# Performance work log

Hardware: AMD Instinct MI355X
Metric: run time of the kernel (lower is better)

## Reference

```python
import jax, jax.numpy as jnp
import numpy as np

NUM_GEMMS = 64      # local experts (num_gemms)
IN_SIZE = 2048      # input_size == config.hidden_size (column parallel)
OUT_SIZE = 1408     # per-expert output width
TOTAL_TOKENS = 32768


def setup_inputs() -> dict:
    key = jax.random.key(0)
    kx, kw = jax.random.split(key)
    x = jax.random.normal(kx, (TOTAL_TOKENS, IN_SIZE), dtype=jnp.float32)
    # torch params are [output_size, input_size] per expert -> stack to [E, out, in]
    W = jax.random.normal(kw, (NUM_GEMMS, OUT_SIZE, IN_SIZE), dtype=jnp.float32) * 0.02
    # uneven per-expert row splits, sum == TOTAL_TOKENS (avg 512, alternating 256/768)
    m_splits = jnp.array([256, 768] * (NUM_GEMMS // 2), dtype=jnp.int32)
    return {"x": x, "W": W, "m_splits": m_splits}


def reference(x, W, m_splits):
    # original: original_weight = cat([w.t() for w in weights]) -> [E*in, out]
    # column mode: view(E, hidden, -1) -> [E, in, out]; gmm over row splits.
    w = jnp.transpose(W, (0, 2, 1))  # [E, in, out]
    splits = np.asarray(m_splits)    # row splits are static metadata of the grouped GEMM
    offs = np.concatenate([[0], np.cumsum(splits)])
    # grouped GEMM: out[rows_of_e] = x[rows_of_e] @ w[e]; loop is over the fixed expert set
    outs = [x[offs[e]:offs[e + 1]] @ w[e] for e in range(w.shape[0])]
    return jnp.concatenate(outs, axis=0)  # [total_tokens, out]
```

## Files before the change

kernel.cpp:

```cpp
#include <hip/hip_runtime.h>
#include <hip/hip_bf16.h>

#define E_ 64
#define K_ 2048
#define N_ 1408
#define BM 256
#define BN 128
#define BK 32
#define NK (K_ / BK)
#define NTHREADS 512
#define NTILE (N_ / BN)
#define LDSA (BM * BK * 2)
#define LDSB (BN * BK * 2)
#define LDSBUF (LDSA + LDSB)
#define GRID_ 2112

using f32x4  = __attribute__((ext_vector_type(4))) float;
using bf16x8 = __attribute__((ext_vector_type(8))) short;

#define BAR() asm volatile("s_waitcnt lgkmcnt(0)\n\ts_barrier" ::: "memory")

__device__ __forceinline__ short f2b(float f) {
  __hip_bfloat16 h = __float2bfloat16(f);
  return __builtin_bit_cast(short, h);
}

__global__ void build_meta(const int* __restrict__ m_splits, int* __restrict__ meta) {
  const int e = threadIdx.x;
  const int m = m_splits[e];
  const int mt = (m + BM - 1) / BM;
  int sm = m, smt = mt;
#pragma unroll
  for (int d = 1; d < 64; d <<= 1) {
    const int vm = __shfl_up(sm, d);
    const int vt = __shfl_up(smt, d);
    if (e >= d) { sm += vm; smt += vt; }
  }
  meta[1 + e] = smt - mt;
  meta[66 + e] = sm - m;
  if (e == 63) { meta[1 + 64] = smt; meta[0] = smt * NTILE; }
}

struct Stage { f32x4 a[2][2]; f32x4 b[2]; };

__global__ __launch_bounds__(NTHREADS, 2) void gemm_grouped(
    const float* __restrict__ x, const float* __restrict__ W,
    const int* __restrict__ m_splits, const int* __restrict__ meta,
    float* __restrict__ out) {
  __shared__ char smem[2 * LDSBUF];

  const int J = meta[0];
  const int xcd = blockIdx.x & 7;
  const int pos = blockIdx.x >> 3;
  const int q = J >> 3, r = J & 7;
  if (pos >= q + (xcd < r ? 1 : 0)) return;
  const int jidx = xcd * q + min(xcd, r) + pos;

  int lo = 0, hi = 64;
  while (hi - lo > 1) {
    const int mid = (lo + hi) >> 1;
    if (meta[1 + mid] * NTILE <= jidx) lo = mid; else hi = mid;
  }
  const int e = lo;
  const int mt_e = meta[1 + e + 1] - meta[1 + e];
  const int rem = jidx - meta[1 + e] * NTILE;
  const int nt = rem / mt_e;
  const int t  = rem - nt * mt_e;
  const int m_e = m_splits[e];
  const int row0 = meta[66 + e] + t * BM;
  const int nrows = min(BM, m_e - t * BM);
  const int n0 = nt * BN;

  const int tid  = threadIdx.x;
  const int lane = tid & 63;
  const int w    = tid >> 6;
  const int wm   = w >> 1;
  const int wn   = w & 1;

  const int strow = tid >> 2;
  const int skc8  = (tid & 3) * 8;
  const int kcb   = (tid & 3) * 16;

  const float* xrow = x + (size_t)row0 * K_;
  const float* wrow = W + ((size_t)e * N_ + (size_t)n0) * K_;
  const f32x4 zero4 = {0.f, 0.f, 0.f, 0.f};

  auto load_tiles = [&](int kt, Stage& st) {
    const int kbase = kt * BK + skc8;
#pragma unroll
    for (int c = 0; c < 2; ++c) {
      const int rr = c * 128 + strow;
      if (rr < nrows) {
        const float* pp = xrow + (size_t)rr * K_ + kbase;
        st.a[c][0] = *(const f32x4*)pp;
        st.a[c][1] = *(const f32x4*)(pp + 4);
      } else { st.a[c][0] = zero4; st.a[c][1] = zero4; }
    }
    const float* qq = wrow + (size_t)strow * K_ + kbase;
    st.b[0] = *(const f32x4*)qq;
    st.b[1] = *(const f32x4*)(qq + 4);
  };

  auto write_lds = [&](int buf, const Stage& st) {
    const int base = buf * LDSBUF;
#pragma unroll
    for (int c = 0; c < 2; ++c) {
      const int rr = c * 128 + strow;
      const int off = rr * 64 + (kcb ^ (((rr >> 1) & 3) << 4));
      bf16x8 v;
#pragma unroll
      for (int i = 0; i < 4; ++i) { v[i] = f2b(st.a[c][0][i]); v[i + 4] = f2b(st.a[c][1][i]); }
      *(bf16x8*)(smem + base + off) = v;
    }
    {
      const int rr = strow;
      const int off = rr * 64 + (kcb ^ (((rr >> 1) & 3) << 4));
      bf16x8 v;
#pragma unroll
      for (int i = 0; i < 4; ++i) { v[i] = f2b(st.b[0][i]); v[i + 4] = f2b(st.b[1][i]); }
      *(bf16x8*)(smem + base + LDSA + off) = v;
    }
  };

  f32x4 acc[4][4];
#pragma unroll
  for (int i = 0; i < 4; ++i)
#pragma unroll
    for (int j = 0; j < 4; ++j) acc[i][j] = zero4;

  const int arow0 = wm * 64 + (lane & 15);
  const int brow0 = wn * 64 + (lane & 15);
  const int kslot = (lane >> 4) * 16;

  auto compute = [&](int buf) {
    const int base = buf * LDSBUF;
    bf16x8 af[4], bfr[4];
#pragma unroll
    for (int i = 0; i < 4; ++i) {
      const int rr = arow0 + i * 16;
      af[i] = *(const bf16x8*)(smem + base + rr * 64 + (kslot ^ (((rr >> 1) & 3) << 4)));
    }
#pragma unroll
    for (int j = 0; j < 4; ++j) {
      const int rr = brow0 + j * 16;
      bfr[j] = *(const bf16x8*)(smem + base + LDSA + rr * 64 + (kslot ^ (((rr >> 1) & 3) << 4)));
    }
#pragma unroll
    for (int i = 0; i < 4; ++i)
#pragma unroll
      for (int j = 0; j < 4; ++j)
        acc[i][j] = __builtin_amdgcn_mfma_f32_16x16x32_bf16(af[i], bfr[j], acc[i][j], 0, 0, 0);
  };

  Stage sA;
  load_tiles(0, sA);
  write_lds(0, sA);
  int cur = 0;
  for (int kt = 0; kt < NK; ++kt) {
    if (kt + 1 < NK) load_tiles(kt + 1, sA);
    BAR();
    compute(cur);
    if (kt + 1 < NK) write_lds(cur ^ 1, sA);
    cur ^= 1;
  }

  const int crow = wm * 64 + (lane >> 4) * 4;
  const int ccol = n0 + wn * 64 + (lane & 15);
#pragma unroll
  for (int i = 0; i < 4; ++i) {
#pragma unroll
    for (int rr = 0; rr < 4; ++rr) {
      const int lr = crow + i * 16 + rr;
      if (lr < nrows) {
#pragma unroll
        for (int j = 0; j < 4; ++j)
          out[(size_t)(row0 + lr) * N_ + ccol + j * 16] = acc[i][j][rr];
      }
    }
  }
}

extern "C" void kernel_launch(void* const* d_in, const int* in_sizes, int n_in,
                              void* d_out, int out_size, void* d_ws, size_t ws_size,
                              hipStream_t stream) {
  const float* x        = (const float*)d_in[0];
  const float* W        = (const float*)d_in[1];
  const int*   m_splits = (const int*)d_in[2];
  float*       out      = (float*)d_out;

  int* meta = (int*)d_ws;

  build_meta<<<1, 64, 0, stream>>>(m_splits, meta);
  gemm_grouped<<<GRID_, NTHREADS, 0, stream>>>(x, W, m_splits, meta, out);
}
```

Measured before the change: 385.2 us.

## Shrink M tile to 128 and remap warps to a 2x4 grid

Measured after the change: 449.6 us. 16.7% more time.

```diff
diff --git a/kernel.cpp b/kernel.cpp
--- a/kernel.cpp
+++ b/kernel.cpp
@@ -4,7 +4,7 @@
 #define E_ 64
 #define K_ 2048
 #define N_ 1408
-#define BM 256
+#define BM 128
 #define BN 128
 #define BK 32
 #define NK (K_ / BK)
@@ -13,7 +13,7 @@
 #define LDSA (BM * BK * 2)
 #define LDSB (BN * BK * 2)
 #define LDSBUF (LDSA + LDSB)
-#define GRID_ 2112
+#define GRID_ 3520
 
 using f32x4  = __attribute__((ext_vector_type(4))) float;
 using bf16x8 = __attribute__((ext_vector_type(8))) short;
@@ -41,9 +41,9 @@
   if (e == 63) { meta[1 + 64] = smt; meta[0] = smt * NTILE; }
 }
 
-struct Stage { f32x4 a[2][2]; f32x4 b[2]; };
+struct Stage { f32x4 a[2]; f32x4 b[2]; };
 
-__global__ __launch_bounds__(NTHREADS, 2) void gemm_grouped(
+__global__ __launch_bounds__(NTHREADS, 6) void gemm_grouped(
     const float* __restrict__ x, const float* __restrict__ W,
     const int* __restrict__ m_splits, const int* __restrict__ meta,
     float* __restrict__ out) {
@@ -74,8 +74,8 @@
   const int tid  = threadIdx.x;
   const int lane = tid & 63;
   const int w    = tid >> 6;
-  const int wm   = w >> 1;
-  const int wn   = w & 1;
+  const int wm   = w >> 2;
+  const int wn   = w & 3;
 
   const int strow = tid >> 2;
   const int skc8  = (tid & 3) * 8;
@@ -87,15 +87,11 @@
 
   auto load_tiles = [&](int kt, Stage& st) {
     const int kbase = kt * BK + skc8;
-#pragma unroll
-    for (int c = 0; c < 2; ++c) {
-      const int rr = c * 128 + strow;
-      if (rr < nrows) {
-        const float* pp = xrow + (size_t)rr * K_ + kbase;
-        st.a[c][0] = *(const f32x4*)pp;
-        st.a[c][1] = *(const f32x4*)(pp + 4);
-      } else { st.a[c][0] = zero4; st.a[c][1] = zero4; }
-    }
+    if (strow < nrows) {
+      const float* pp = xrow + (size_t)strow * K_ + kbase;
+      st.a[0] = *(const f32x4*)pp;
+      st.a[1] = *(const f32x4*)(pp + 4);
+    } else { st.a[0] = zero4; st.a[1] = zero4; }
     const float* qq = wrow + (size_t)strow * K_ + kbase;
     st.b[0] = *(const f32x4*)qq;
     st.b[1] = *(const f32x4*)(qq + 4);
@@ -103,53 +99,42 @@
 
   auto write_lds = [&](int buf, const Stage& st) {
     const int base = buf * LDSBUF;
+    const int off = strow * 64 + (kcb ^ (((strow >> 1) & 3) << 4));
+    bf16x8 va, vb;
 #pragma unroll
-    for (int c = 0; c < 2; ++c) {
-      const int rr = c * 128 + strow;
-      const int off = rr * 64 + (kcb ^ (((rr >> 1) & 3) << 4));
-      bf16x8 v;
+    for (int i = 0; i < 4; ++i) { va[i] = f2b(st.a[0][i]); va[i + 4] = f2b(st.a[1][i]); }
 #pragma unroll
-      for (int i = 0; i < 4; ++i) { v[i] = f2b(st.a[c][0][i]); v[i + 4] = f2b(st.a[c][1][i]); }
-      *(bf16x8*)(smem + base + off) = v;
-    }
-    {
-      const int rr = strow;
-      const int off = rr * 64 + (kcb ^ (((rr >> 1) & 3) << 4));
-      bf16x8 v;
-#pragma unroll
-      for (int i = 0; i < 4; ++i) { v[i] = f2b(st.b[0][i]); v[i + 4] = f2b(st.b[1][i]); }
-      *(bf16x8*)(smem + base + LDSA + off) = v;
-    }
+    for (int i = 0; i < 4; ++i) { vb[i] = f2b(st.b[0][i]); vb[i + 4] = f2b(st.b[1][i]); }
+    *(bf16x8*)(smem + base + off)        = va;
+    *(bf16x8*)(smem + base + LDSA + off) = vb;
   };
 
-  f32x4 acc[4][4];
+  f32x4 acc[4][2];
 #pragma unroll
   for (int i = 0; i < 4; ++i)
 #pragma unroll
-    for (int j = 0; j < 4; ++j) acc[i][j] = zero4;
+    for (int j = 0; j < 2; ++j) acc[i][j] = zero4;
 
   const int arow0 = wm * 64 + (lane & 15);
-  const int brow0 = wn * 64 + (lane & 15);
+  const int brow0 = wn * 32 + (lane & 15);
   const int kslot = (lane >> 4) * 16;
 
   auto compute = [&](int buf) {
     const int base = buf * LDSBUF;
-    bf16x8 af[4], bfr[4];
+    bf16x8 bf0, bf1;
+    {
+      const int r0b = brow0;
+      const int r1b = brow0 + 16;
+      bf0 = *(const bf16x8*)(smem + base + LDSA + r0b * 64 + (kslot ^ (((r0b >> 1) & 3) << 4)));
+      bf1 = *(const bf16x8*)(smem + base + LDSA + r1b * 64 + (kslot ^ (((r1b >> 1) & 3) << 4)));
+    }
 #pragma unroll
     for (int i = 0; i < 4; ++i) {
       const int rr = arow0 + i * 16;
-      af[i] = *(const bf16x8*)(smem + base + rr * 64 + (kslot ^ (((rr >> 1) & 3) << 4)));
+      bf16x8 af = *(const bf16x8*)(smem + base + rr * 64 + (kslot ^ (((rr >> 1) & 3) << 4)));
+      acc[i][0] = __builtin_amdgcn_mfma_f32_16x16x32_bf16(af, bf0, acc[i][0], 0, 0, 0);
+      acc[i][1] = __builtin_amdgcn_mfma_f32_16x16x32_bf16(af, bf1, acc[i][1], 0, 0, 0);
     }
-#pragma unroll
-    for (int j = 0; j < 4; ++j) {
-      const int rr = brow0 + j * 16;
-      bfr[j] = *(const bf16x8*)(smem + base + LDSA + rr * 64 + (kslot ^ (((rr >> 1) & 3) << 4)));
-    }
-#pragma unroll
-    for (int i = 0; i < 4; ++i)
-#pragma unroll
-      for (int j = 0; j < 4; ++j)
-        acc[i][j] = __builtin_amdgcn_mfma_f32_16x16x32_bf16(af[i], bfr[j], acc[i][j], 0, 0, 0);
   };
 
   Stage sA;
@@ -165,7 +150,7 @@
   }
 
   const int crow = wm * 64 + (lane >> 4) * 4;
-  const int ccol = n0 + wn * 64 + (lane & 15);
+  const int ccol = n0 + wn * 32 + (lane & 15);
 #pragma unroll
   for (int i = 0; i < 4; ++i) {
 #pragma unroll
@@ -173,7 +158,7 @@
       const int lr = crow + i * 16 + rr;
       if (lr < nrows) {
 #pragma unroll
-        for (int j = 0; j < 4; ++j)
+        for (int j = 0; j < 2; ++j)
           out[(size_t)(row0 + lr) * N_ + ccol + j * 16] = acc[i][j][rr];
       }
     }
```
